# Performance work log

Measured on AMD Instinct MI355X. Metric: run time of the kernel, lower is better.

Reference implementation:

```python
import jax, jax.numpy as jnp
import numpy as np

MODEL_DIM = 1024
TOTAL_DIM = 1024
N_HEADS = 16
HEAD_DIM = TOTAL_DIM // N_HEADS


def setup_inputs() -> dict:
    key = jax.random.key(0)
    k1, k2, k3 = jax.random.split(key, 3)
    query = jax.random.normal(k1, (2, 2048, MODEL_DIM), dtype=jnp.float32)
    # nn.Linear(model_dim, 3*total_dim, bias=False): store as [in, out] for x @ W
    W_in = jax.random.normal(k2, (MODEL_DIM, 3 * TOTAL_DIM), dtype=jnp.float32) / np.sqrt(MODEL_DIM)
    W_out = jax.random.normal(k3, (TOTAL_DIM, MODEL_DIM), dtype=jnp.float32) / np.sqrt(TOTAL_DIM)
    return {"query": query, "W_in": W_in, "W_out": W_out}


def reference(query, W_in, W_out):
    B, S, _ = query.shape
    qkv = query @ W_in                      # [B, S, 3*D]
    q, k, v = jnp.split(qkv, 3, axis=-1)    # each [B, S, D]

    def to_heads(t):
        return t.reshape(B, S, N_HEADS, HEAD_DIM).transpose(0, 2, 1, 3)  # [B,H,S,d]

    q, k, v = to_heads(q), to_heads(k), to_heads(v)
    scale = 1.0 / np.sqrt(HEAD_DIM).astype(np.float32)
    scores = jnp.einsum('bhqd,bhkd->bhqk', q, k) * scale  # [B,H,S,S]
    causal = jnp.tril(jnp.ones((S, S), dtype=bool))
    scores = jnp.where(causal, scores, jnp.finfo(scores.dtype).min)
    probs = jax.nn.softmax(scores, axis=-1)
    attn = jnp.einsum('bhqk,bhkd->bhqd', probs, v)        # [B,H,S,d]
    attn = attn.transpose(0, 2, 1, 3).reshape(B, S, TOTAL_DIM)
    return attn @ W_out                     # [B, S, model_dim]
```

## Files before the change

kernel.cpp:

```cpp
#include <hip/hip_runtime.h>


typedef __bf16 bf16x8 __attribute__((ext_vector_type(8)));
typedef float f32x4 __attribute__((ext_vector_type(4)));
typedef int i32x4 __attribute__((ext_vector_type(4)));

#define B_   2
#define S_   2048
#define DM   1024
#define NH   16
#define HD   64
#define N3   3072
#define M_   4096

#define SCALE_LOG2E 0.180336884f

__device__ __forceinline__ unsigned short f2bf(float f) {
  unsigned int u = __float_as_uint(f);
  u += 0x7fffu + ((u >> 16) & 1u);
  return (unsigned short)(u >> 16);
}

__device__ __forceinline__ void gload_lds16(void* lds, const void* g) {
  __builtin_amdgcn_global_load_lds(
      (__attribute__((address_space(1))) void*)g,
      (__attribute__((address_space(3))) void*)lds, 16, 0, 0);
}

__global__ __launch_bounds__(256) void f32_to_bf16_vec(
    const float4* __restrict__ in, unsigned short* __restrict__ out, int n4) {
  int i = blockIdx.x * 256 + threadIdx.x;
  if (i < n4) {
    float4 v = in[i];
    ushort4 o;
    o.x = f2bf(v.x); o.y = f2bf(v.y); o.z = f2bf(v.z); o.w = f2bf(v.w);
    *(ushort4*)(&out[(size_t)i * 4]) = o;
  }
}

__global__ __launch_bounds__(256) void transpose_f32_bf16(
    const float* __restrict__ in, unsigned short* __restrict__ out, int R, int C) {
  __shared__ float tile[32][33];
  const int tx = threadIdx.x, ty = threadIdx.y;
  const int x = blockIdx.x * 32 + tx;
  const int y0 = blockIdx.y * 32;
#pragma unroll
  for (int j = 0; j < 32; j += 8)
    tile[ty + j][tx] = in[(size_t)(y0 + ty + j) * C + x];
  __syncthreads();
  const int ox = y0 + tx;
  const int oy0 = blockIdx.x * 32;
#pragma unroll
  for (int j = 0; j < 32; j += 8)
    out[(size_t)(oy0 + ty + j) * R + ox] = f2bf(tile[tx][ty + j]);
}

__global__ __launch_bounds__(256) void gemm_qkv(
    const unsigned short* __restrict__ A,
    const unsigned short* __restrict__ Bt,
    unsigned short* __restrict__ qkv2,
    unsigned short* __restrict__ vT) {
  __shared__ __align__(16) unsigned short a_sm[128 * 64];
  __shared__ __align__(16) unsigned short b_sm[128 * 64];
  const int id = blockIdx.x;
  const int xcd = id & 7, j8 = id >> 3;
  const int ct = xcd * 3 + (j8 % 3);
  const int rt = j8 / 3;
  const bool isv = ct >= 16;
  const int row0 = rt * 128, col0 = ct * 128;

  const int tid = threadIdx.x;
  const int lane = tid & 63, wave = tid >> 6;
  const int quad = lane >> 4, l15 = lane & 15;
  const int sw = l15 & 7;
  const int wm = (wave >> 1) * 64, wn = (wave & 1) * 64;

  f32x4 acc[4][4];
#pragma unroll
  for (int i = 0; i < 4; i++)
#pragma unroll
    for (int j = 0; j < 4; j++) acc[i][j] = (f32x4){0.f, 0.f, 0.f, 0.f};

  const int c_src = ((tid & 7) ^ ((tid >> 3) & 7)) * 8;
  const int r_st = tid >> 3;
  const unsigned short* Ab = A + (size_t)(row0 + r_st) * DM + c_src;
  const unsigned short* Bb = Bt + (size_t)(col0 + r_st) * DM + c_src;

  for (int k0 = 0; k0 < DM; k0 += 64) {
    __syncthreads();
#pragma unroll
    for (int rnd = 0; rnd < 4; rnd++) {
      gload_lds16(&a_sm[tid * 8 + rnd * 2048], Ab + k0 + (size_t)rnd * 32 * DM);
      gload_lds16(&b_sm[tid * 8 + rnd * 2048], Bb + k0 + (size_t)rnd * 32 * DM);
    }
    __syncthreads();

    bf16x8 af[4][2], bfr[4][2];
#pragma unroll
    for (int i = 0; i < 4; i++)
#pragma unroll
      for (int h = 0; h < 2; h++) {
        const int ch = ((h * 4 + quad) ^ sw) << 3;
        af[i][h]  = *(const bf16x8*)&a_sm[(wm + i * 16 + l15) * 64 + ch];
        bfr[i][h] = *(const bf16x8*)&b_sm[(wn + i * 16 + l15) * 64 + ch];
      }
    if (!isv) {
#pragma unroll
      for (int i = 0; i < 4; i++)
#pragma unroll
        for (int j = 0; j < 4; j++)
#pragma unroll
          for (int h = 0; h < 2; h++)
            acc[i][j] = __builtin_amdgcn_mfma_f32_16x16x32_bf16(af[i][h], bfr[j][h], acc[i][j], 0, 0, 0);
    } else {
#pragma unroll
      for (int i = 0; i < 4; i++)
#pragma unroll
        for (int j = 0; j < 4; j++)
#pragma unroll
          for (int h = 0; h < 2; h++)
            acc[i][j] = __builtin_amdgcn_mfma_f32_16x16x32_bf16(bfr[i][h], af[j][h], acc[i][j], 0, 0, 0);
    }
  }

  if (!isv) {
#pragma unroll
    for (int i = 0; i < 4; i++)
#pragma unroll
      for (int j = 0; j < 4; j++)
#pragma unroll
        for (int r = 0; r < 4; r++) {
          const int row = row0 + wm + i * 16 + quad * 4 + r;
          const int col = col0 + wn + j * 16 + l15;
          qkv2[(size_t)row * 2048 + col] = f2bf(acc[i][j][r]);
        }
  } else {
    const int head = ((col0 - 2048) >> 6) + (wn >> 6);
    const int bidx = row0 >> 11;
    const int s_base = (row0 & 2047) + wm;
#pragma unroll
    for (int i = 0; i < 4; i++)
#pragma unroll
      for (int j = 0; j < 4; j++)
#pragma unroll
        for (int r = 0; r < 4; r++) {
          const int d = i * 16 + quad * 4 + r;
          const int s = s_base + j * 16 + l15;
          vT[((size_t)((bidx * NH + head) * HD + d)) * S_ + s] = f2bf(acc[i][j][r]);
        }
  }
}

__global__ __launch_bounds__(256) void attn_fused4(
    const unsigned short* __restrict__ qkv2,
    const unsigned short* __restrict__ vT,
    unsigned short* __restrict__ attnout) {
  const int h = blockIdx.y, b = blockIdx.z;
  const int qt = (b == 0) ? blockIdx.x : (31 - blockIdx.x);
  const int tid = threadIdx.x;
  const int lane = tid & 63, wave = tid >> 6;
  const int quad = lane >> 4, l15 = lane & 15;
  const int sw = l15 & 7;

  __shared__ __align__(16) unsigned short k_sm[2 * 4096];
  __shared__ __align__(16) unsigned short vt_sm[2 * 4096];

  const int Q0 = qt * 64;
  const int qrow = Q0 + wave * 16 + l15;
  const int wrow0 = Q0 + wave * 16;

  bf16x8 qf[2];
  {
    const unsigned short* qp = qkv2 + (size_t)(b * S_ + qrow) * 2048 + h * HD + quad * 8;
    qf[0] = *(const bf16x8*)qp;
    qf[1] = *(const bf16x8*)(qp + 32);
  }

  f32x4 o[4];
#pragma unroll
  for (int n = 0; n < 4; n++) o[n] = (f32x4){0.f, 0.f, 0.f, 0.f};
  float lsum = 0.f;

  const int r0s = tid >> 3;
  const int gch = ((tid & 7) ^ (r0s & 7)) * 8;
  const unsigned short* kgb = qkv2 + (size_t)(b * S_ + r0s) * 2048 + DM + h * HD + gch;
  const unsigned short* vgb = vT + (size_t)((b * NH + h) * HD + r0s) * S_ + gch;

  const int addrA = (((quad * 2) & 3) * 16 + l15) * 4;
  const int addrB = (((quad * 2 + 1) & 3) * 16 + l15) * 4;

  const int nt = qt + 1;
  gload_lds16(&k_sm[tid * 8], kgb);
  gload_lds16(&k_sm[2048 + tid * 8], kgb + (size_t)32 * 2048);
  gload_lds16(&vt_sm[tid * 8], vgb);
  gload_lds16(&vt_sm[2048 + tid * 8], vgb + (size_t)32 * S_);

  for (int t = 0; t < nt; t++) {
    __syncthreads();
    if (t + 1 < nt) {
      const int nb = ((t + 1) & 1) * 4096;
      const unsigned short* kg = kgb + (size_t)(t + 1) * 64 * 2048;
      const unsigned short* vg = vgb + (t + 1) * 64;
      gload_lds16(&k_sm[nb + tid * 8], kg);
      gload_lds16(&k_sm[nb + 2048 + tid * 8], kg + (size_t)32 * 2048);
      gload_lds16(&vt_sm[nb + tid * 8], vg);
      gload_lds16(&vt_sm[nb + 2048 + tid * 8], vg + (size_t)32 * S_);
    }

    const unsigned short* kb = &k_sm[(t & 1) * 4096];
    const unsigned short* vb = &vt_sm[(t & 1) * 4096];

    f32x4 s[4];
#pragma unroll
    for (int mb = 0; mb < 4; mb++) s[mb] = (f32x4){0.f, 0.f, 0.f, 0.f};
#pragma unroll
    for (int mb = 0; mb < 4; mb++) {
      const int ro = (mb * 16 + l15) * 64;
      bf16x8 kf0 = *(const bf16x8*)&kb[ro + ((quad ^ sw) << 3)];
      bf16x8 kf1 = *(const bf16x8*)&kb[ro + (((4 + quad) ^ sw) << 3)];
      s[mb] = __builtin_amdgcn_mfma_f32_16x16x32_bf16(kf0, qf[0], s[mb], 0, 0, 0);
      s[mb] = __builtin_amdgcn_mfma_f32_16x16x32_bf16(kf1, qf[1], s[mb], 0, 0, 0);
    }

    if (t < qt) {
#pragma unroll
      for (int mb = 0; mb < 4; mb++)
#pragma unroll
        for (int r = 0; r < 4; r++)
          s[mb][r] = exp2f(s[mb][r] * SCALE_LOG2E);
    } else {
      const int kb0 = t * 64 + quad * 4;
#pragma unroll
      for (int mb = 0; mb < 4; mb++)
#pragma unroll
        for (int r = 0; r < 4; r++) {
          const float e = exp2f(s[mb][r] * SCALE_LOG2E);
          s[mb][r] = (kb0 + mb * 16 + r <= qrow) ? e : 0.f;
        }
    }
#pragma unroll
    for (int mb = 0; mb < 4; mb++)
      lsum += (s[mb][0] + s[mb][1]) + (s[mb][2] + s[mb][3]);

    int pk[4][2];
#pragma unroll
    for (int mb = 0; mb < 4; mb++) {
      const unsigned u0 = __float_as_uint(s[mb][0]) + 0x8000u;
      const unsigned u1 = __float_as_uint(s[mb][1]) + 0x8000u;
      const unsigned u2 = __float_as_uint(s[mb][2]) + 0x8000u;
      const unsigned u3 = __float_as_uint(s[mb][3]) + 0x8000u;
      pk[mb][0] = (int)__builtin_amdgcn_perm(u1, u0, 0x07060302u);
      pk[mb][1] = (int)__builtin_amdgcn_perm(u3, u2, 0x07060302u);
    }

    const bool hi = quad >= 2;
#pragma unroll
    for (int ks = 0; ks < 2; ks++) {
      const int m0 = 2 * ks, m1 = m0 + 1;
      const int f0a = __builtin_amdgcn_ds_bpermute(addrA, pk[m0][0]);
      const int f0b = __builtin_amdgcn_ds_bpermute(addrA, pk[m1][0]);
      const int f1a = __builtin_amdgcn_ds_bpermute(addrA, pk[m0][1]);
      const int f1b = __builtin_amdgcn_ds_bpermute(addrA, pk[m1][1]);
      const int f2a = __builtin_amdgcn_ds_bpermute(addrB, pk[m0][0]);
      const int f2b = __builtin_amdgcn_ds_bpermute(addrB, pk[m1][0]);
      const int f3a = __builtin_amdgcn_ds_bpermute(addrB, pk[m0][1]);
      const int f3b = __builtin_amdgcn_ds_bpermute(addrB, pk[m1][1]);
      i32x4 fr;
      fr.x = hi ? f0b : f0a;
      fr.y = hi ? f1b : f1a;
      fr.z = hi ? f2b : f2a;
      fr.w = hi ? f3b : f3a;
      const bf16x8 pfrag = __builtin_bit_cast(bf16x8, fr);
#pragma unroll
      for (int mb = 0; mb < 4; mb++) {
        const int ro = (mb * 16 + l15) * 64;
        bf16x8 vf = *(const bf16x8*)&vb[ro + (((ks * 4 + quad) ^ sw) << 3)];
        o[mb] = __builtin_amdgcn_mfma_f32_16x16x32_bf16(vf, pfrag, o[mb], 0, 0, 0);
      }
    }
  }

  float l = lsum;
  l += __shfl_xor(l, 16);
  l += __shfl_xor(l, 32);
  const float inv = 1.0f / l;
  const size_t grow = (size_t)(b * S_ + qrow);
#pragma unroll
  for (int mb = 0; mb < 4; mb++) {
    ushort4 w;
    w.x = f2bf(o[mb][0] * inv);
    w.y = f2bf(o[mb][1] * inv);
    w.z = f2bf(o[mb][2] * inv);
    w.w = f2bf(o[mb][3] * inv);
    *(ushort4*)&attnout[grow * DM + h * HD + mb * 16 + quad * 4] = w;
  }
}

__global__ __launch_bounds__(256) void gemm_out(
    const unsigned short* __restrict__ A,
    const unsigned short* __restrict__ Bt,
    float* __restrict__ C) {
  __shared__ __align__(16) unsigned short a_sm[128 * 32];
  __shared__ __align__(16) unsigned short b_sm[64 * 32];
  const int id = blockIdx.x;
  const int ctile = id & 15, rtile = id >> 4;
  const int row0 = rtile * 128, col0 = ctile * 64;

  const int tid = threadIdx.x;
  const int lane = tid & 63, wave = tid >> 6;
  const int quad = lane >> 4, l15 = lane & 15;
  const int wm = wave * 32;

  f32x4 acc[2][4];
#pragma unroll
  for (int i = 0; i < 2; i++)
#pragma unroll
    for (int j = 0; j < 4; j++) acc[i][j] = (f32x4){0.f, 0.f, 0.f, 0.f};

  const int rA = tid >> 2, cA = (tid & 3) * 8;

  for (int k0 = 0; k0 < DM; k0 += 32) {
    __syncthreads();
    gload_lds16(&a_sm[tid * 8],        &A[(size_t)(row0 + rA) * DM + k0 + cA]);
    gload_lds16(&a_sm[tid * 8 + 2048], &A[(size_t)(row0 + rA + 64) * DM + k0 + cA]);
    gload_lds16(&b_sm[tid * 8],        &Bt[(size_t)(col0 + rA) * DM + k0 + cA]);
    __syncthreads();

    bf16x8 af[2], bf[4];
#pragma unroll
    for (int i = 0; i < 2; i++)
      af[i] = *(const bf16x8*)&a_sm[(wm + i * 16 + l15) * 32 + quad * 8];
#pragma unroll
    for (int j = 0; j < 4; j++)
      bf[j] = *(const bf16x8*)&b_sm[(j * 16 + l15) * 32 + quad * 8];
#pragma unroll
    for (int i = 0; i < 2; i++)
#pragma unroll
      for (int j = 0; j < 4; j++)
        acc[i][j] = __builtin_amdgcn_mfma_f32_16x16x32_bf16(af[i], bf[j], acc[i][j], 0, 0, 0);
  }

#pragma unroll
  for (int i = 0; i < 2; i++)
#pragma unroll
    for (int j = 0; j < 4; j++)
#pragma unroll
      for (int r = 0; r < 4; r++) {
        const int row = row0 + wm + i * 16 + quad * 4 + r;
        const int col = col0 + j * 16 + l15;
        C[(size_t)row * DM + col] = acc[i][j][r];
      }
}

extern "C" void kernel_launch(void* const* d_in, const int* in_sizes, int n_in,
                              void* d_out, int out_size, void* d_ws, size_t ws_size,
                              hipStream_t stream) {
  const float* query = (const float*)d_in[0];
  const float* w_in  = (const float*)d_in[1];
  const float* w_out = (const float*)d_in[2];
  float* out = (float*)d_out;

  char* ws = (char*)d_ws;
  unsigned short* qbf     = (unsigned short*)(ws);
  unsigned short* w_in_t  = (unsigned short*)(ws + 8388608);
  unsigned short* w_out_t = (unsigned short*)(ws + 14680064);
  unsigned short* qkv2    = (unsigned short*)(ws + 16777216);
  unsigned short* vT      = (unsigned short*)(ws + 33554432);
  unsigned short* attn    = (unsigned short*)(ws + 41943040);

  f32_to_bf16_vec<<<dim3(M_ * DM / 1024), dim3(256), 0, stream>>>(
      (const float4*)query, qbf, M_ * DM / 4);
  transpose_f32_bf16<<<dim3(N3 / 32, DM / 32), dim3(32, 8), 0, stream>>>(w_in, w_in_t, DM, N3);
  transpose_f32_bf16<<<dim3(DM / 32, DM / 32), dim3(32, 8), 0, stream>>>(w_out, w_out_t, DM, DM);
  gemm_qkv<<<dim3(768), dim3(256), 0, stream>>>(qbf, w_in_t, qkv2, vT);
  attn_fused4<<<dim3(32, NH, B_), dim3(256), 0, stream>>>(qkv2, vT, attn);
  gemm_out<<<dim3(512), dim3(256), 0, stream>>>(attn, w_out_t, out);
}
```

Baseline: 215.2 us.

## Merge weight transposes, shrink QKV K-tile, widen attention blocks, swizzle out-GEMM LDS

The two weight-transpose launches are merged into one grid. The QKV GEMM K-step drops from 64 to 32, which halves its LDS footprint and adds a launch-bounds occupancy hint of 4. The attention kernel now runs 512 threads over 128 query rows, so each K/V tile loaded into LDS serves twice as many rows. It double-buffers pairs of 64-key tiles and skips tiles that are fully masked per wave. The output GEMM gets an XOR swizzle on its LDS reads to cut bank conflicts, at the cost of more barriers per K in the QKV GEMM.

```diff
diff --git a/kernel.cpp b/kernel.cpp
--- a/kernel.cpp
+++ b/kernel.cpp
@@ -38,30 +38,37 @@
   }
 }
 
-__global__ __launch_bounds__(256) void transpose_f32_bf16(
-    const float* __restrict__ in, unsigned short* __restrict__ out, int R, int C) {
+__global__ __launch_bounds__(256) void transpose_weights(
+    const float* __restrict__ w_in, const float* __restrict__ w_out,
+    unsigned short* __restrict__ w_in_t, unsigned short* __restrict__ w_out_t) {
   __shared__ float tile[32][33];
+  const int bx = blockIdx.x;
+  const float* in;
+  unsigned short* out;
+  int C, x0;
+  if (bx < 96) { in = w_in;  out = w_in_t;  C = N3; x0 = bx * 32; }
+  else         { in = w_out; out = w_out_t; C = DM; x0 = (bx - 96) * 32; }
   const int tx = threadIdx.x, ty = threadIdx.y;
-  const int x = blockIdx.x * 32 + tx;
+  const int x = x0 + tx;
   const int y0 = blockIdx.y * 32;
 #pragma unroll
   for (int j = 0; j < 32; j += 8)
     tile[ty + j][tx] = in[(size_t)(y0 + ty + j) * C + x];
   __syncthreads();
   const int ox = y0 + tx;
-  const int oy0 = blockIdx.x * 32;
+  const int oy0 = x0;
 #pragma unroll
   for (int j = 0; j < 32; j += 8)
-    out[(size_t)(oy0 + ty + j) * R + ox] = f2bf(tile[tx][ty + j]);
-}
-
-__global__ __launch_bounds__(256) void gemm_qkv(
+    out[(size_t)(oy0 + ty + j) * DM + ox] = f2bf(tile[tx][ty + j]);
+}
+
+__global__ __launch_bounds__(256, 4) void gemm_qkv(
     const unsigned short* __restrict__ A,
     const unsigned short* __restrict__ Bt,
     unsigned short* __restrict__ qkv2,
     unsigned short* __restrict__ vT) {
-  __shared__ __align__(16) unsigned short a_sm[128 * 64];
-  __shared__ __align__(16) unsigned short b_sm[128 * 64];
+  __shared__ __align__(16) unsigned short a_sm[128 * 32];
+  __shared__ __align__(16) unsigned short b_sm[128 * 32];
   const int id = blockIdx.x;
   const int xcd = id & 7, j8 = id >> 3;
   const int ct = xcd * 3 + (j8 % 3);
@@ -72,7 +79,6 @@
   const int tid = threadIdx.x;
   const int lane = tid & 63, wave = tid >> 6;
   const int quad = lane >> 4, l15 = lane & 15;
-  const int sw = l15 & 7;
   const int wm = (wave >> 1) * 64, wn = (wave & 1) * 64;
 
   f32x4 acc[4][4];
@@ -81,45 +87,38 @@
 #pragma unroll
     for (int j = 0; j < 4; j++) acc[i][j] = (f32x4){0.f, 0.f, 0.f, 0.f};
 
-  const int c_src = ((tid & 7) ^ ((tid >> 3) & 7)) * 8;
-  const int r_st = tid >> 3;
+  const int r_st = tid >> 2;
+  const int c_src = ((tid & 3) ^ (r_st & 3)) * 8;
   const unsigned short* Ab = A + (size_t)(row0 + r_st) * DM + c_src;
   const unsigned short* Bb = Bt + (size_t)(col0 + r_st) * DM + c_src;
-
-  for (int k0 = 0; k0 < DM; k0 += 64) {
-    __syncthreads();
-#pragma unroll
-    for (int rnd = 0; rnd < 4; rnd++) {
-      gload_lds16(&a_sm[tid * 8 + rnd * 2048], Ab + k0 + (size_t)rnd * 32 * DM);
-      gload_lds16(&b_sm[tid * 8 + rnd * 2048], Bb + k0 + (size_t)rnd * 32 * DM);
+  const int rch = (quad ^ (l15 & 3)) << 3;
+
+  for (int k0 = 0; k0 < DM; k0 += 32) {
+    __syncthreads();
+    gload_lds16(&a_sm[tid * 8],        Ab + k0);
+    gload_lds16(&a_sm[tid * 8 + 2048], Ab + k0 + (size_t)64 * DM);
+    gload_lds16(&b_sm[tid * 8],        Bb + k0);
+    gload_lds16(&b_sm[tid * 8 + 2048], Bb + k0 + (size_t)64 * DM);
+    __syncthreads();
+
+    bf16x8 af[4], bfr[4];
+#pragma unroll
+    for (int i = 0; i < 4; i++) {
+      af[i]  = *(const bf16x8*)&a_sm[(wm + i * 16 + l15) * 32 + rch];
+      bfr[i] = *(const bf16x8*)&b_sm[(wn + i * 16 + l15) * 32 + rch];
     }
-    __syncthreads();
-
-    bf16x8 af[4][2], bfr[4][2];
-#pragma unroll
-    for (int i = 0; i < 4; i++)
-#pragma unroll
-      for (int h = 0; h < 2; h++) {
-        const int ch = ((h * 4 + quad) ^ sw) << 3;
-        af[i][h]  = *(const bf16x8*)&a_sm[(wm + i * 16 + l15) * 64 + ch];
-        bfr[i][h] = *(const bf16x8*)&b_sm[(wn + i * 16 + l15) * 64 + ch];
-      }
     if (!isv) {
 #pragma unroll
       for (int i = 0; i < 4; i++)
 #pragma unroll
         for (int j = 0; j < 4; j++)
-#pragma unroll
-          for (int h = 0; h < 2; h++)
-            acc[i][j] = __builtin_amdgcn_mfma_f32_16x16x32_bf16(af[i][h], bfr[j][h], acc[i][j], 0, 0, 0);
+          acc[i][j] = __builtin_amdgcn_mfma_f32_16x16x32_bf16(af[i], bfr[j], acc[i][j], 0, 0, 0);
     } else {
 #pragma unroll
       for (int i = 0; i < 4; i++)
 #pragma unroll
         for (int j = 0; j < 4; j++)
-#pragma unroll
-          for (int h = 0; h < 2; h++)
-            acc[i][j] = __builtin_amdgcn_mfma_f32_16x16x32_bf16(bfr[i][h], af[j][h], acc[i][j], 0, 0, 0);
+          acc[i][j] = __builtin_amdgcn_mfma_f32_16x16x32_bf16(bfr[i], af[j], acc[i][j], 0, 0, 0);
     }
   }
 
@@ -151,21 +150,21 @@
   }
 }
 
-__global__ __launch_bounds__(256) void attn_fused4(
+__global__ __launch_bounds__(512, 4) void attn_fused5(
     const unsigned short* __restrict__ qkv2,
     const unsigned short* __restrict__ vT,
     unsigned short* __restrict__ attnout) {
   const int h = blockIdx.y, b = blockIdx.z;
-  const int qt = (b == 0) ? blockIdx.x : (31 - blockIdx.x);
+  const int qt = (b == 0) ? blockIdx.x : (15 - blockIdx.x);
   const int tid = threadIdx.x;
   const int lane = tid & 63, wave = tid >> 6;
   const int quad = lane >> 4, l15 = lane & 15;
   const int sw = l15 & 7;
 
-  __shared__ __align__(16) unsigned short k_sm[2 * 4096];
-  __shared__ __align__(16) unsigned short vt_sm[2 * 4096];
-
-  const int Q0 = qt * 64;
+  __shared__ __align__(16) unsigned short k_sm[4 * 4096];
+  __shared__ __align__(16) unsigned short vt_sm[4 * 4096];
+
+  const int Q0 = qt * 128;
   const int qrow = Q0 + wave * 16 + l15;
   const int wrow0 = Q0 + wave * 16;
 
@@ -189,93 +188,99 @@
   const int addrA = (((quad * 2) & 3) * 16 + l15) * 4;
   const int addrB = (((quad * 2 + 1) & 3) * 16 + l15) * 4;
 
-  const int nt = qt + 1;
-  gload_lds16(&k_sm[tid * 8], kgb);
-  gload_lds16(&k_sm[2048 + tid * 8], kgb + (size_t)32 * 2048);
-  gload_lds16(&vt_sm[tid * 8], vgb);
-  gload_lds16(&vt_sm[2048 + tid * 8], vgb + (size_t)32 * S_);
-
-  for (int t = 0; t < nt; t++) {
-    __syncthreads();
-    if (t + 1 < nt) {
-      const int nb = ((t + 1) & 1) * 4096;
-      const unsigned short* kg = kgb + (size_t)(t + 1) * 64 * 2048;
-      const unsigned short* vg = vgb + (t + 1) * 64;
-      gload_lds16(&k_sm[nb + tid * 8], kg);
-      gload_lds16(&k_sm[nb + 2048 + tid * 8], kg + (size_t)32 * 2048);
-      gload_lds16(&vt_sm[nb + tid * 8], vg);
-      gload_lds16(&vt_sm[nb + 2048 + tid * 8], vg + (size_t)32 * S_);
+  const int nt = 2 * qt + 2;
+  gload_lds16(&k_sm[tid * 8],          kgb);
+  gload_lds16(&k_sm[4096 + tid * 8],   kgb + (size_t)64 * 2048);
+  gload_lds16(&vt_sm[tid * 8],         vgb);
+  gload_lds16(&vt_sm[4096 + tid * 8],  vgb + 64);
+
+  for (int tt = 0; tt < nt; tt += 2) {
+    __syncthreads();
+    const int bufo = ((tt >> 1) & 1) * 8192;
+    if (tt + 2 < nt) {
+      const int nb = 8192 - bufo;
+      const unsigned short* kg = kgb + (size_t)(tt + 2) * 64 * 2048;
+      const unsigned short* vg = vgb + (tt + 2) * 64;
+      gload_lds16(&k_sm[nb + tid * 8],         kg);
+      gload_lds16(&k_sm[nb + 4096 + tid * 8],  kg + (size_t)64 * 2048);
+      gload_lds16(&vt_sm[nb + tid * 8],        vg);
+      gload_lds16(&vt_sm[nb + 4096 + tid * 8], vg + 64);
     }
 
-    const unsigned short* kb = &k_sm[(t & 1) * 4096];
-    const unsigned short* vb = &vt_sm[(t & 1) * 4096];
-
-    f32x4 s[4];
-#pragma unroll
-    for (int mb = 0; mb < 4; mb++) s[mb] = (f32x4){0.f, 0.f, 0.f, 0.f};
-#pragma unroll
-    for (int mb = 0; mb < 4; mb++) {
-      const int ro = (mb * 16 + l15) * 64;
-      bf16x8 kf0 = *(const bf16x8*)&kb[ro + ((quad ^ sw) << 3)];
-      bf16x8 kf1 = *(const bf16x8*)&kb[ro + (((4 + quad) ^ sw) << 3)];
-      s[mb] = __builtin_amdgcn_mfma_f32_16x16x32_bf16(kf0, qf[0], s[mb], 0, 0, 0);
-      s[mb] = __builtin_amdgcn_mfma_f32_16x16x32_bf16(kf1, qf[1], s[mb], 0, 0, 0);
-    }
-
-    if (t < qt) {
-#pragma unroll
-      for (int mb = 0; mb < 4; mb++)
-#pragma unroll
-        for (int r = 0; r < 4; r++)
-          s[mb][r] = exp2f(s[mb][r] * SCALE_LOG2E);
-    } else {
-      const int kb0 = t * 64 + quad * 4;
-#pragma unroll
-      for (int mb = 0; mb < 4; mb++)
-#pragma unroll
-        for (int r = 0; r < 4; r++) {
-          const float e = exp2f(s[mb][r] * SCALE_LOG2E);
-          s[mb][r] = (kb0 + mb * 16 + r <= qrow) ? e : 0.f;
-        }
-    }
-#pragma unroll
-    for (int mb = 0; mb < 4; mb++)
-      lsum += (s[mb][0] + s[mb][1]) + (s[mb][2] + s[mb][3]);
-
-    int pk[4][2];
-#pragma unroll
-    for (int mb = 0; mb < 4; mb++) {
-      const unsigned u0 = __float_as_uint(s[mb][0]) + 0x8000u;
-      const unsigned u1 = __float_as_uint(s[mb][1]) + 0x8000u;
-      const unsigned u2 = __float_as_uint(s[mb][2]) + 0x8000u;
-      const unsigned u3 = __float_as_uint(s[mb][3]) + 0x8000u;
-      pk[mb][0] = (int)__builtin_amdgcn_perm(u1, u0, 0x07060302u);
-      pk[mb][1] = (int)__builtin_amdgcn_perm(u3, u2, 0x07060302u);
-    }
-
-    const bool hi = quad >= 2;
-#pragma unroll
-    for (int ks = 0; ks < 2; ks++) {
-      const int m0 = 2 * ks, m1 = m0 + 1;
-      const int f0a = __builtin_amdgcn_ds_bpermute(addrA, pk[m0][0]);
-      const int f0b = __builtin_amdgcn_ds_bpermute(addrA, pk[m1][0]);
-      const int f1a = __builtin_amdgcn_ds_bpermute(addrA, pk[m0][1]);
-      const int f1b = __builtin_amdgcn_ds_bpermute(addrA, pk[m1][1]);
-      const int f2a = __builtin_amdgcn_ds_bpermute(addrB, pk[m0][0]);
-      const int f2b = __builtin_amdgcn_ds_bpermute(addrB, pk[m1][0]);
-      const int f3a = __builtin_amdgcn_ds_bpermute(addrB, pk[m0][1]);
-      const int f3b = __builtin_amdgcn_ds_bpermute(addrB, pk[m1][1]);
-      i32x4 fr;
-      fr.x = hi ? f0b : f0a;
-      fr.y = hi ? f1b : f1a;
-      fr.z = hi ? f2b : f2a;
-      fr.w = hi ? f3b : f3a;
-      const bf16x8 pfrag = __builtin_bit_cast(bf16x8, fr);
+#pragma unroll
+    for (int u = 0; u < 2; u++) {
+      const int t = tt + u;
+      if (t * 64 > wrow0 + 15) continue;
+      const unsigned short* kb = &k_sm[bufo + u * 4096];
+      const unsigned short* vb = &vt_sm[bufo + u * 4096];
+
+      f32x4 s[4];
+#pragma unroll
+      for (int mb = 0; mb < 4; mb++) s[mb] = (f32x4){0.f, 0.f, 0.f, 0.f};
 #pragma unroll
       for (int mb = 0; mb < 4; mb++) {
         const int ro = (mb * 16 + l15) * 64;
-        bf16x8 vf = *(const bf16x8*)&vb[ro + (((ks * 4 + quad) ^ sw) << 3)];
-        o[mb] = __builtin_amdgcn_mfma_f32_16x16x32_bf16(vf, pfrag, o[mb], 0, 0, 0);
+        bf16x8 kf0 = *(const bf16x8*)&kb[ro + ((quad ^ sw) << 3)];
+        bf16x8 kf1 = *(const bf16x8*)&kb[ro + (((4 + quad) ^ sw) << 3)];
+        s[mb] = __builtin_amdgcn_mfma_f32_16x16x32_bf16(kf0, qf[0], s[mb], 0, 0, 0);
+        s[mb] = __builtin_amdgcn_mfma_f32_16x16x32_bf16(kf1, qf[1], s[mb], 0, 0, 0);
+      }
+
+      if (t * 64 + 63 <= wrow0) {
+#pragma unroll
+        for (int mb = 0; mb < 4; mb++)
+#pragma unroll
+          for (int r = 0; r < 4; r++)
+            s[mb][r] = exp2f(s[mb][r] * SCALE_LOG2E);
+      } else {
+        const int kb0 = t * 64 + quad * 4;
+#pragma unroll
+        for (int mb = 0; mb < 4; mb++)
+#pragma unroll
+          for (int r = 0; r < 4; r++) {
+            const float e = exp2f(s[mb][r] * SCALE_LOG2E);
+            s[mb][r] = (kb0 + mb * 16 + r <= qrow) ? e : 0.f;
+          }
+      }
+#pragma unroll
+      for (int mb = 0; mb < 4; mb++)
+        lsum += (s[mb][0] + s[mb][1]) + (s[mb][2] + s[mb][3]);
+
+      int pk[4][2];
+#pragma unroll
+      for (int mb = 0; mb < 4; mb++) {
+        const unsigned u0 = __float_as_uint(s[mb][0]) + 0x8000u;
+        const unsigned u1 = __float_as_uint(s[mb][1]) + 0x8000u;
+        const unsigned u2 = __float_as_uint(s[mb][2]) + 0x8000u;
+        const unsigned u3 = __float_as_uint(s[mb][3]) + 0x8000u;
+        pk[mb][0] = (int)__builtin_amdgcn_perm(u1, u0, 0x07060302u);
+        pk[mb][1] = (int)__builtin_amdgcn_perm(u3, u2, 0x07060302u);
+      }
+
+      const bool hi = quad >= 2;
+#pragma unroll
+      for (int ks = 0; ks < 2; ks++) {
+        const int m0 = 2 * ks, m1 = m0 + 1;
+        const int f0a = __builtin_amdgcn_ds_bpermute(addrA, pk[m0][0]);
+        const int f0b = __builtin_amdgcn_ds_bpermute(addrA, pk[m1][0]);
+        const int f1a = __builtin_amdgcn_ds_bpermute(addrA, pk[m0][1]);
+        const int f1b = __builtin_amdgcn_ds_bpermute(addrA, pk[m1][1]);
+        const int f2a = __builtin_amdgcn_ds_bpermute(addrB, pk[m0][0]);
+        const int f2b = __builtin_amdgcn_ds_bpermute(addrB, pk[m1][0]);
+        const int f3a = __builtin_amdgcn_ds_bpermute(addrB, pk[m0][1]);
+        const int f3b = __builtin_amdgcn_ds_bpermute(addrB, pk[m1][1]);
+        i32x4 fr;
+        fr.x = hi ? f0b : f0a;
+        fr.y = hi ? f1b : f1a;
+        fr.z = hi ? f2b : f2a;
+        fr.w = hi ? f3b : f3a;
+        const bf16x8 pfrag = __builtin_bit_cast(bf16x8, fr);
+#pragma unroll
+        for (int mb = 0; mb < 4; mb++) {
+          const int ro = (mb * 16 + l15) * 64;
+          bf16x8 vf = *(const bf16x8*)&vb[ro + (((ks * 4 + quad) ^ sw) << 3)];
+          o[mb] = __builtin_amdgcn_mfma_f32_16x16x32_bf16(vf, pfrag, o[mb], 0, 0, 0);
+        }
       }
     }
   }
@@ -317,7 +322,9 @@
 #pragma unroll
     for (int j = 0; j < 4; j++) acc[i][j] = (f32x4){0.f, 0.f, 0.f, 0.f};
 
-  const int rA = tid >> 2, cA = (tid & 3) * 8;
+  const int rA = tid >> 2;
+  const int cA = ((tid & 3) ^ (rA & 3)) * 8;
+  const int rch = (quad ^ (l15 & 3)) << 3;
 
   for (int k0 = 0; k0 < DM; k0 += 32) {
     __syncthreads();
@@ -329,10 +336,10 @@
     bf16x8 af[2], bf[4];
 #pragma unroll
     for (int i = 0; i < 2; i++)
-      af[i] = *(const bf16x8*)&a_sm[(wm + i * 16 + l15) * 32 + quad * 8];
+      af[i] = *(const bf16x8*)&a_sm[(wm + i * 16 + l15) * 32 + rch];
 #pragma unroll
     for (int j = 0; j < 4; j++)
-      bf[j] = *(const bf16x8*)&b_sm[(j * 16 + l15) * 32 + quad * 8];
+      bf[j] = *(const bf16x8*)&b_sm[(j * 16 + l15) * 32 + rch];
 #pragma unroll
     for (int i = 0; i < 2; i++)
 #pragma unroll
@@ -370,9 +377,8 @@
 
   f32_to_bf16_vec<<<dim3(M_ * DM / 1024), dim3(256), 0, stream>>>(
       (const float4*)query, qbf, M_ * DM / 4);
-  transpose_f32_bf16<<<dim3(N3 / 32, DM / 32), dim3(32, 8), 0, stream>>>(w_in, w_in_t, DM, N3);
-  transpose_f32_bf16<<<dim3(DM / 32, DM / 32), dim3(32, 8), 0, stream>>>(w_out, w_out_t, DM, DM);
+  transpose_weights<<<dim3(128, 32), dim3(32, 8), 0, stream>>>(w_in, w_out, w_in_t, w_out_t);
   gemm_qkv<<<dim3(768), dim3(256), 0, stream>>>(qbf, w_in_t, qkv2, vT);
-  attn_fused4<<<dim3(32, NH, B_), dim3(256), 0, stream>>>(qkv2, vT, attn);
+  attn_fused5<<<dim3(16, NH, B_), dim3(512), 0, stream>>>(qkv2, vT, attn);
   gemm_out<<<dim3(512), dim3(256), 0, stream>>>(attn, w_out_t, out);
 }
```

Measured after the change: 360.5 us. 1.67x slower.
